# Kernel tuning notes

Measured on AMD Instinct MI355X. Metric: run time of the kernel, lower is better.

The kernel has to match this reference:

```python
import jax, jax.numpy as jnp
import numpy as np

B, S, H = 4, 8192, 1024


def setup_inputs() -> dict:
    key = jax.random.key(0)
    kq, kk, kv, k1, k2, k3, k4 = jax.random.split(key, 7)
    residual_init_factor = 1.0
    return {
        "q": jax.random.normal(kq, (B, S, H), dtype=jnp.float32),
        "k": jax.random.normal(kk, (B, S, H), dtype=jnp.float32),
        "v": jax.random.normal(kv, (B, S, H), dtype=jnp.float32),
        "w_q": 0.01 * jax.random.normal(k1, (H, H), dtype=jnp.float32),
        "w_k": 0.01 * jax.random.normal(k2, (H, H), dtype=jnp.float32),
        "w_v": 0.01 * jax.random.normal(k3, (H, H), dtype=jnp.float32),
        "w_p": 0.01 * residual_init_factor * jax.random.normal(k4, (H, H), dtype=jnp.float32),
    }


def reference(q, k, v, w_q, w_k, w_v, w_p):
    # Projections: [B,S,H] @ [H,H]
    emb_q = jnp.einsum("bsh,hd->bsd", q, w_q)
    emb_k = jnp.einsum("bsh,hd->bsd", k, w_k)
    emb_v = jnp.einsum("bsh,hd->bsd", v, w_v)
    # AFT-simple: per-channel exponential-weighted causal prefix average
    k_exp = jnp.exp(emb_k)
    k_exp_prefix = jnp.cumsum(k_exp, axis=1)
    k_exp_v_prefix = jnp.cumsum(k_exp * emb_v, axis=1)
    y = jax.nn.sigmoid(emb_q) * (k_exp_v_prefix / k_exp_prefix)
    return jnp.einsum("bsh,hd->bsd", y, w_p)
```

## Files before the change

kernel.cpp:

```cpp
#include <hip/hip_runtime.h>
#include <hip/hip_bf16.h>
#include <cstdint>

#define AS_GLOBAL __attribute__((address_space(1)))
#define AS_LDS    __attribute__((address_space(3)))

typedef __attribute__((ext_vector_type(8))) short bf16x8;
typedef __attribute__((ext_vector_type(8))) unsigned short u16x8;
typedef __attribute__((ext_vector_type(4))) float f32x4;

static __device__ __forceinline__ ushort f2bf(float x) {
    union { float f; uint32_t u; } c;
    c.f = x;
    uint32_t u = c.u;
    u += 0x7fffu + ((u >> 16) & 1u);
    return (ushort)(u >> 16);
}
static __device__ __forceinline__ float bf2f(ushort u) {
    union { uint32_t i; float f; } c;
    c.i = ((uint32_t)u) << 16;
    return c.f;
}

static __device__ __forceinline__ void gload_lds16(const void* g, void* l) {
    __builtin_amdgcn_global_load_lds(
        (const AS_GLOBAL uint32_t*)(uintptr_t)g,
        (AS_LDS uint32_t*)(uint32_t)(uintptr_t)l,
        16, 0, 0);
}

__global__ __launch_bounds__(256)
void cvt_f32_bf16(const float4* __restrict__ in, u16x8* __restrict__ out, int n8) {
    int i = blockIdx.x * 256 + threadIdx.x;
    int stride = gridDim.x * 256;
    for (; i < n8; i += stride) {
        float4 a = in[i * 2], b = in[i * 2 + 1];
        u16x8 o;
        o[0] = f2bf(a.x); o[1] = f2bf(a.y); o[2] = f2bf(a.z); o[3] = f2bf(a.w);
        o[4] = f2bf(b.x); o[5] = f2bf(b.y); o[6] = f2bf(b.z); o[7] = f2bf(b.w);
        out[i] = o;
    }
}

__global__ __launch_bounds__(256)
void transpose4_to_bf16(const float* __restrict__ w0, const float* __restrict__ w1,
                        const float* __restrict__ w2, const float* __restrict__ w3,
                        ushort* __restrict__ t0, ushort* __restrict__ t1,
                        ushort* __restrict__ t2, ushort* __restrict__ t3) {
    const int K = 1024, N = 1024;
    __shared__ float tile[32][33];
    const float* w; ushort* wt;
    switch (blockIdx.z) {
        case 0: w = w0; wt = t0; break;
        case 1: w = w1; wt = t1; break;
        case 2: w = w2; wt = t2; break;
        default: w = w3; wt = t3; break;
    }
    int bn = blockIdx.x * 32;
    int bk = blockIdx.y * 32;
    int tx = threadIdx.x & 31, ty = threadIdx.x >> 5;
    #pragma unroll
    for (int i = 0; i < 32; i += 8)
        tile[ty + i][tx] = w[(size_t)(bk + ty + i) * N + bn + tx];
    __syncthreads();
    #pragma unroll
    for (int i = 0; i < 32; i += 8)
        wt[(size_t)(bn + ty + i) * K + bk + tx] = f2bf(tile[tx][ty + i]);
}

template<int EPI, int OUT_BF>
__global__ __launch_bounds__(512, 2)
void gemm8p(const ushort* __restrict__ A, const ushort* __restrict__ Bt,
            void* __restrict__ Cv) {
    constexpr int K = 1024, N = 1024;
    __shared__ alignas(16) ushort sA[3][256 * 64];
    __shared__ alignas(16) ushort sB[3][128 * 64];
    const int tid  = threadIdx.x;
    const int wid  = tid >> 6;
    const int lane = tid & 63;
    const int wr = wid >> 1, wc = wid & 1;
    const int lr = lane & 15;
    const int kb = lane >> 4;
    const int x7 = lr & 7;

    const int wg = blockIdx.x;
    const int xcd = wg & 7, local = wg >> 3;
    const int bm = xcd * 16 + (local >> 3);
    const int bn = local & 7;
    const int m0 = bm * 256, n0 = bn * 128;

    f32x4 acc[4][4] = {};
    bf16x8 af[4][2];
    bf16x8 bv[2][2];

    auto stageA2 = [&](int tile, int buf, int j0) {
        const int kt0 = tile * 64;
        #pragma unroll
        for (int j = 0; j < 2; j++) {
            int c = (j0 + j) * 512 + tid;
            int r = c >> 3, p = c & 7;
            int s = p ^ (r & 7);
            gload_lds16(A + (size_t)(m0 + r) * K + kt0 + s * 8, &sA[buf][c * 8]);
        }
    };
    auto stageB1 = [&](int tile, int buf, int j) {
        const int kt0 = tile * 64;
        int c = j * 512 + tid;
        int r = c >> 3, p = c & 7;
        int s = p ^ (r & 7);
        gload_lds16(Bt + (size_t)(n0 + r) * K + kt0 + s * 8, &sB[buf][c * 8]);
    };
    auto readA = [&](int buf) {
        #pragma unroll
        for (int m = 0; m < 4; m++)
            #pragma unroll
            for (int kh = 0; kh < 2; kh++)
                af[m][kh] = *(const bf16x8*)&sA[buf][(wr * 64 + m * 16 + lr) * 64
                                                    + ((kh * 4 + kb) ^ x7) * 8];
    };
    auto readB = [&](int buf, int nq) {
        #pragma unroll
        for (int n = 0; n < 2; n++)
            #pragma unroll
            for (int kh = 0; kh < 2; kh++)
                bv[n][kh] = *(const bf16x8*)&sB[buf][(wc * 64 + nq * 32 + n * 16 + lr) * 64
                                                    + ((kh * 4 + kb) ^ x7) * 8];
    };
    auto mfma16 = [&](int nq) {
        #pragma unroll
        for (int m = 0; m < 4; m++)
            #pragma unroll
            for (int n = 0; n < 2; n++) {
                acc[m][nq * 2 + n] = __builtin_amdgcn_mfma_f32_16x16x32_bf16(
                    af[m][0], bv[n][0], acc[m][nq * 2 + n], 0, 0, 0);
                acc[m][nq * 2 + n] = __builtin_amdgcn_mfma_f32_16x16x32_bf16(
                    af[m][1], bv[n][1], acc[m][nq * 2 + n], 0, 0, 0);
            }
    };

    stageA2(0, 0, 0); stageA2(0, 0, 2); stageB1(0, 0, 0); stageB1(0, 0, 1);
    stageA2(1, 1, 0); stageA2(1, 1, 2); stageB1(1, 1, 0); stageB1(1, 1, 1);
    asm volatile("s_waitcnt vmcnt(6)" ::: "memory");
    __builtin_amdgcn_s_barrier();
    asm volatile("" ::: "memory");

    for (int t = 0; t < 16; t++) {
        const int b  = t % 3;
        const int b2 = (t + 2) % 3;
        const bool st = (t < 14);
        readA(b);
        readB(b, 0);
        if (st) { stageA2(t + 2, b2, 0); stageB1(t + 2, b2, 0); }
        asm volatile("" ::: "memory");
        __builtin_amdgcn_s_barrier();
        asm volatile("s_waitcnt lgkmcnt(0)" ::: "memory");
        __builtin_amdgcn_s_setprio(1);
        mfma16(0);
        __builtin_amdgcn_s_setprio(0);
        asm volatile("" ::: "memory");
        __builtin_amdgcn_s_barrier();
        asm volatile("" ::: "memory");
        readB(b, 1);
        if (st) { stageA2(t + 2, b2, 2); stageB1(t + 2, b2, 1); }
        asm volatile("" ::: "memory");
        __builtin_amdgcn_s_barrier();
        asm volatile("s_waitcnt lgkmcnt(0)" ::: "memory");
        __builtin_amdgcn_s_setprio(1);
        mfma16(1);
        __builtin_amdgcn_s_setprio(0);
        if (t < 14)       asm volatile("s_waitcnt vmcnt(6)" ::: "memory");
        else if (t == 14) asm volatile("s_waitcnt vmcnt(0)" ::: "memory");
        asm volatile("" ::: "memory");
        __builtin_amdgcn_s_barrier();
        asm volatile("" ::: "memory");
    }

    float*  Cf = (float*)Cv;
    ushort* Cb = (ushort*)Cv;
    #pragma unroll
    for (int m = 0; m < 4; m++) {
        #pragma unroll
        for (int n = 0; n < 4; n++) {
            #pragma unroll
            for (int r = 0; r < 4; r++) {
                int row = m0 + wr * 64 + m * 16 + (lane >> 4) * 4 + r;
                int col = n0 + wc * 64 + n * 16 + (lane & 15);
                float v = acc[m][n][r];
                if (EPI == 1) v = 1.0f / (1.0f + __expf(-v));
                else if (EPI == 2) v = __expf(v);
                size_t idx = (size_t)row * N + col;
                if (OUT_BF) Cb[idx] = f2bf(v);
                else        Cf[idx] = v;
            }
        }
    }
}

__global__ __launch_bounds__(256)
void scan_partials(const ushort* __restrict__ ke, const ushort* __restrict__ ev,
                   float* __restrict__ pke, float* __restrict__ pkv) {
    const int H = 1024, S = 8192, CHUNK = 32, BH = 4096;
    int c  = blockIdx.x * 2 + (threadIdx.x >> 7);
    int h0 = (threadIdx.x & 127) * 8;
    int b  = blockIdx.y;
    size_t base = ((size_t)b * S + (size_t)c * CHUNK) * H + h0;
    float se[8] = {}, sv[8] = {};
    for (int s = 0; s < CHUNK; s++) {
        u16x8 e8 = *(const u16x8*)(ke + base + (size_t)s * H);
        u16x8 v8 = *(const u16x8*)(ev + base + (size_t)s * H);
        #pragma unroll
        for (int i = 0; i < 8; i++) {
            float e = bf2f(e8[i]);
            se[i] += e;
            sv[i] += e * bf2f(v8[i]);
        }
    }
    size_t p = (size_t)c * BH + b * H + h0;
    *(float4*)(pke + p)     = make_float4(se[0], se[1], se[2], se[3]);
    *(float4*)(pke + p + 4) = make_float4(se[4], se[5], se[6], se[7]);
    *(float4*)(pkv + p)     = make_float4(sv[0], sv[1], sv[2], sv[3]);
    *(float4*)(pkv + p + 4) = make_float4(sv[4], sv[5], sv[6], sv[7]);
}

__global__ __launch_bounds__(256)
void scan_offsets(float* __restrict__ pke, float* __restrict__ pkv, int nch, int BH) {
    int i = blockIdx.x * blockDim.x + threadIdx.x;
    if (i >= BH) return;
    float rke = 0.f, rkv = 0.f;
    #pragma unroll 8
    for (int c = 0; c < nch; c++) {
        size_t idx = (size_t)c * BH + i;
        float a = pke[idx], b = pkv[idx];
        pke[idx] = rke; pkv[idx] = rkv;
        rke += a; rkv += b;
    }
}

__global__ __launch_bounds__(256)
void scan_final(const ushort* __restrict__ ke, const ushort* __restrict__ ev,
                const ushort* __restrict__ sq,
                const float* __restrict__ pke, const float* __restrict__ pkv,
                ushort* __restrict__ ybf) {
    const int H = 1024, S = 8192, CHUNK = 32, BH = 4096;
    int c  = blockIdx.x * 2 + (threadIdx.x >> 7);
    int h0 = (threadIdx.x & 127) * 8;
    int b  = blockIdx.y;
    size_t p = (size_t)c * BH + b * H + h0;
    float rke[8], rkv[8];
    *(float4*)(rke)     = *(const float4*)(pke + p);
    *(float4*)(rke + 4) = *(const float4*)(pke + p + 4);
    *(float4*)(rkv)     = *(const float4*)(pkv + p);
    *(float4*)(rkv + 4) = *(const float4*)(pkv + p + 4);
    size_t base = ((size_t)b * S + (size_t)c * CHUNK) * H + h0;
    for (int s = 0; s < CHUNK; s++) {
        size_t idx = base + (size_t)s * H;
        u16x8 e8 = *(const u16x8*)(ke + idx);
        u16x8 v8 = *(const u16x8*)(ev + idx);
        u16x8 q8 = *(const u16x8*)(sq + idx);
        u16x8 o;
        #pragma unroll
        for (int i = 0; i < 8; i++) {
            float e = bf2f(e8[i]);
            rke[i] += e;
            rkv[i] += e * bf2f(v8[i]);
            o[i] = f2bf(bf2f(q8[i]) * (rkv[i] / rke[i]));
        }
        *(u16x8*)(ybf + idx) = o;
    }
}

extern "C" void kernel_launch(void* const* d_in, const int* in_sizes, int n_in,
                              void* d_out, int out_size, void* d_ws, size_t ws_size,
                              hipStream_t stream) {
    const float* q   = (const float*)d_in[0];
    const float* k   = (const float*)d_in[1];
    const float* v   = (const float*)d_in[2];
    const float* w_q = (const float*)d_in[3];
    const float* w_k = (const float*)d_in[4];
    const float* w_v = (const float*)d_in[5];
    const float* w_p = (const float*)d_in[6];
    float* out = (float*)d_out;

    const int B = 4, S = 8192, H = 1024;
    const int M = B * S;
    const size_t MH = (size_t)M * H;
    const int NCH = 256;
    const int BH = B * H;

    char* ws = (char*)d_ws;
    size_t off = 0;
    auto alloc = [&](size_t bytes) -> char* {
        char* p = ws + off;
        off += (bytes + 255) & ~(size_t)255;
        return p;
    };
    ushort* abuf = (ushort*)alloc(MH * 2);
    ushort* wqt  = (ushort*)alloc((size_t)H * H * 2);
    ushort* wkt  = (ushort*)alloc((size_t)H * H * 2);
    ushort* wvt  = (ushort*)alloc((size_t)H * H * 2);
    ushort* wpt  = (ushort*)alloc((size_t)H * H * 2);
    ushort* sqb  = (ushort*)alloc(MH * 2);
    ushort* keb  = (ushort*)alloc(MH * 2);
    ushort* evb  = (ushort*)alloc(MH * 2);
    float*  pke  = (float*)alloc((size_t)NCH * BH * 4);
    float*  pkv  = (float*)alloc((size_t)NCH * BH * 4);

    const int ngg = (M / 256) * (H / 128);
    dim3 tg(H / 32, H / 32, 4);
    dim3 gs(NCH / 2, B);
    const int n8 = (int)(MH / 8);

    transpose4_to_bf16<<<tg, 256, 0, stream>>>(w_q, w_k, w_v, w_p, wqt, wkt, wvt, wpt);

    cvt_f32_bf16<<<2048, 256, 0, stream>>>((const float4*)q, (u16x8*)abuf, n8);
    gemm8p<1, 1><<<ngg, 512, 0, stream>>>(abuf, wqt, sqb);
    cvt_f32_bf16<<<2048, 256, 0, stream>>>((const float4*)k, (u16x8*)abuf, n8);
    gemm8p<2, 1><<<ngg, 512, 0, stream>>>(abuf, wkt, keb);
    cvt_f32_bf16<<<2048, 256, 0, stream>>>((const float4*)v, (u16x8*)abuf, n8);
    gemm8p<0, 1><<<ngg, 512, 0, stream>>>(abuf, wvt, evb);

    scan_partials<<<gs, 256, 0, stream>>>(keb, evb, pke, pkv);
    scan_offsets<<<BH / 256, 256, 0, stream>>>(pke, pkv, NCH, BH);
    scan_final<<<gs, 256, 0, stream>>>(keb, evb, sqb, pke, pkv, abuf);

    gemm8p<0, 0><<<ngg, 512, 0, stream>>>(abuf, wpt, out);
}
```

Before: 553.8 us.

## Enlarge GEMM block tile to 256x256 with 8-phase double-buffered pipeline

The GEMM block tile grows from 256x128 to 256x256. Each wave now computes a 128x64 output tile with 128 accumulator registers, and the 3-stage LDS ring becomes a 2-stage double buffer organised as quarter tiles. Eight interleaved phases alternate A and B half-tile loads with MFMA work. The aim is to raise arithmetic intensity and cut the number of global and LDS loads per FLOP, at the cost of much higher register pressure (possible spills or lower occupancy with launch_bounds 512,2) and fewer blocks (512 per GEMM).

New measurement: 530.1 us. -4.3%, faster.

```diff
diff --git a/kernel.cpp b/kernel.cpp
--- a/kernel.cpp
+++ b/kernel.cpp
@@ -73,119 +73,151 @@
 void gemm8p(const ushort* __restrict__ A, const ushort* __restrict__ Bt,
             void* __restrict__ Cv) {
     constexpr int K = 1024, N = 1024;
-    __shared__ alignas(16) ushort sA[3][256 * 64];
-    __shared__ alignas(16) ushort sB[3][128 * 64];
+    __shared__ alignas(16) ushort sA[2][16384];
+    __shared__ alignas(16) ushort sB[2][16384];
     const int tid  = threadIdx.x;
     const int wid  = tid >> 6;
     const int lane = tid & 63;
-    const int wr = wid >> 1, wc = wid & 1;
+    const int wr = wid >> 2, wc = wid & 3;
     const int lr = lane & 15;
     const int kb = lane >> 4;
     const int x7 = lr & 7;
 
     const int wg = blockIdx.x;
     const int xcd = wg & 7, local = wg >> 3;
-    const int bm = xcd * 16 + (local >> 3);
-    const int bn = local & 7;
-    const int m0 = bm * 256, n0 = bn * 128;
-
-    f32x4 acc[4][4] = {};
+    const int bm = xcd * 16 + (local >> 2);
+    const int bn = local & 3;
+    const int m0 = bm * 256, n0 = bn * 256;
+
+    f32x4 acc[8][4] = {};
     bf16x8 af[4][2];
-    bf16x8 bv[2][2];
-
-    auto stageA2 = [&](int tile, int buf, int j0) {
+    bf16x8 bv0[2][2], bv1[2][2];
+
+    auto stageA = [&](int tile, int buf, int mh) {
         const int kt0 = tile * 64;
         #pragma unroll
         for (int j = 0; j < 2; j++) {
-            int c = (j0 + j) * 512 + tid;
-            int r = c >> 3, p = c & 7;
-            int s = p ^ (r & 7);
-            gload_lds16(A + (size_t)(m0 + r) * K + kt0 + s * 8, &sA[buf][c * 8]);
-        }
-    };
-    auto stageB1 = [&](int tile, int buf, int j) {
+            int c = j * 512 + tid;
+            int rl = c >> 3, p = c & 7;
+            int s = p ^ (rl & 7);
+            int gr = (rl >> 6) * 128 + mh * 64 + (rl & 63);
+            gload_lds16(A + (size_t)(m0 + gr) * K + kt0 + s * 8,
+                        &sA[buf][mh * 8192 + c * 8]);
+        }
+    };
+    auto stageB = [&](int tile, int buf, int nh) {
         const int kt0 = tile * 64;
-        int c = j * 512 + tid;
-        int r = c >> 3, p = c & 7;
-        int s = p ^ (r & 7);
-        gload_lds16(Bt + (size_t)(n0 + r) * K + kt0 + s * 8, &sB[buf][c * 8]);
-    };
-    auto readA = [&](int buf) {
+        #pragma unroll
+        for (int j = 0; j < 2; j++) {
+            int c = j * 512 + tid;
+            int cl = c >> 3, p = c & 7;
+            int s = p ^ (cl & 7);
+            int gc = (cl >> 5) * 64 + nh * 32 + (cl & 31);
+            gload_lds16(Bt + (size_t)(n0 + gc) * K + kt0 + s * 8,
+                        &sB[buf][nh * 8192 + c * 8]);
+        }
+    };
+    auto readA = [&](int buf, int mq) {
         #pragma unroll
         for (int m = 0; m < 4; m++)
             #pragma unroll
             for (int kh = 0; kh < 2; kh++)
-                af[m][kh] = *(const bf16x8*)&sA[buf][(wr * 64 + m * 16 + lr) * 64
-                                                    + ((kh * 4 + kb) ^ x7) * 8];
-    };
-    auto readB = [&](int buf, int nq) {
+                af[m][kh] = *(const bf16x8*)&sA[buf][mq * 8192
+                              + (wr * 64 + m * 16 + lr) * 64
+                              + ((kh * 4 + kb) ^ x7) * 8];
+    };
+    auto readB = [&](bf16x8 (&dst)[2][2], int buf, int nq) {
         #pragma unroll
         for (int n = 0; n < 2; n++)
             #pragma unroll
             for (int kh = 0; kh < 2; kh++)
-                bv[n][kh] = *(const bf16x8*)&sB[buf][(wc * 64 + nq * 32 + n * 16 + lr) * 64
-                                                    + ((kh * 4 + kb) ^ x7) * 8];
-    };
-    auto mfma16 = [&](int nq) {
+                dst[n][kh] = *(const bf16x8*)&sB[buf][nq * 8192
+                              + (wc * 32 + n * 16 + lr) * 64
+                              + ((kh * 4 + kb) ^ x7) * 8];
+    };
+    auto mfma16 = [&](bf16x8 (&BV)[2][2], int mq, int nq) {
         #pragma unroll
         for (int m = 0; m < 4; m++)
             #pragma unroll
             for (int n = 0; n < 2; n++) {
-                acc[m][nq * 2 + n] = __builtin_amdgcn_mfma_f32_16x16x32_bf16(
-                    af[m][0], bv[n][0], acc[m][nq * 2 + n], 0, 0, 0);
-                acc[m][nq * 2 + n] = __builtin_amdgcn_mfma_f32_16x16x32_bf16(
-                    af[m][1], bv[n][1], acc[m][nq * 2 + n], 0, 0, 0);
+                acc[mq*4+m][nq*2+n] = __builtin_amdgcn_mfma_f32_16x16x32_bf16(
+                    af[m][0], BV[n][0], acc[mq*4+m][nq*2+n], 0, 0, 0);
+                acc[mq*4+m][nq*2+n] = __builtin_amdgcn_mfma_f32_16x16x32_bf16(
+                    af[m][1], BV[n][1], acc[mq*4+m][nq*2+n], 0, 0, 0);
             }
     };
 
-    stageA2(0, 0, 0); stageA2(0, 0, 2); stageB1(0, 0, 0); stageB1(0, 0, 1);
-    stageA2(1, 1, 0); stageA2(1, 1, 2); stageB1(1, 1, 0); stageB1(1, 1, 1);
-    asm volatile("s_waitcnt vmcnt(6)" ::: "memory");
+#define PHASE(BV, MQ, NQ, READS, STAGES, ENDW) { \
+    READS \
+    STAGES \
+    asm volatile("" ::: "memory"); \
+    __builtin_amdgcn_s_barrier(); \
+    asm volatile("s_waitcnt lgkmcnt(0)" ::: "memory"); \
+    __builtin_amdgcn_s_setprio(1); \
+    mfma16(BV, MQ, NQ); \
+    __builtin_amdgcn_s_setprio(0); \
+    ENDW \
+    asm volatile("" ::: "memory"); \
+    __builtin_amdgcn_s_barrier(); \
+    asm volatile("" ::: "memory"); \
+}
+
+    stageA(0, 0, 0); stageA(0, 0, 1); stageB(0, 0, 0); stageB(0, 0, 1);
+    stageA(1, 1, 0); stageA(1, 1, 1); stageB(1, 1, 0); stageB(1, 1, 1);
+    asm volatile("s_waitcnt vmcnt(0)" ::: "memory");
     __builtin_amdgcn_s_barrier();
     asm volatile("" ::: "memory");
 
-    for (int t = 0; t < 16; t++) {
-        const int b  = t % 3;
-        const int b2 = (t + 2) % 3;
-        const bool st = (t < 14);
-        readA(b);
-        readB(b, 0);
-        if (st) { stageA2(t + 2, b2, 0); stageB1(t + 2, b2, 0); }
-        asm volatile("" ::: "memory");
-        __builtin_amdgcn_s_barrier();
-        asm volatile("s_waitcnt lgkmcnt(0)" ::: "memory");
-        __builtin_amdgcn_s_setprio(1);
-        mfma16(0);
-        __builtin_amdgcn_s_setprio(0);
-        asm volatile("" ::: "memory");
-        __builtin_amdgcn_s_barrier();
-        asm volatile("" ::: "memory");
-        readB(b, 1);
-        if (st) { stageA2(t + 2, b2, 2); stageB1(t + 2, b2, 1); }
-        asm volatile("" ::: "memory");
-        __builtin_amdgcn_s_barrier();
-        asm volatile("s_waitcnt lgkmcnt(0)" ::: "memory");
-        __builtin_amdgcn_s_setprio(1);
-        mfma16(1);
-        __builtin_amdgcn_s_setprio(0);
-        if (t < 14)       asm volatile("s_waitcnt vmcnt(6)" ::: "memory");
-        else if (t == 14) asm volatile("s_waitcnt vmcnt(0)" ::: "memory");
-        asm volatile("" ::: "memory");
-        __builtin_amdgcn_s_barrier();
-        asm volatile("" ::: "memory");
-    }
+    for (int i = 0; i < 8; i++) {
+        const int t = 2 * i;
+        const int bt = t & 1, bt1 = bt ^ 1;
+        PHASE(bv0, 0, 0,
+            { readA(bt, 0); readB(bv0, bt, 0); },
+            { if (i > 0) stageA(t + 1, bt1, 0); },
+            { })
+        PHASE(bv1, 0, 1,
+            { readB(bv1, bt, 1); },
+            { if (i > 0) stageA(t + 1, bt1, 1); },
+            { asm volatile("s_waitcnt vmcnt(8)" ::: "memory"); })
+        PHASE(bv0, 1, 0,
+            { readA(bt, 1); },
+            { if (i < 7) stageB(t + 2, bt, 0); },
+            { })
+        PHASE(bv1, 1, 1,
+            { },
+            { if (i < 7) stageB(t + 2, bt, 1); },
+            { if (i < 7) asm volatile("s_waitcnt vmcnt(6)" ::: "memory");
+              else       asm volatile("s_waitcnt vmcnt(0)" ::: "memory"); })
+        PHASE(bv0, 0, 0,
+            { readA(bt1, 0); readB(bv0, bt1, 0); },
+            { if (i < 7) stageA(t + 2, bt, 0); },
+            { })
+        PHASE(bv1, 0, 1,
+            { readB(bv1, bt1, 1); },
+            { if (i < 7) stageA(t + 2, bt, 1); },
+            { if (i < 7) asm volatile("s_waitcnt vmcnt(8)" ::: "memory"); })
+        PHASE(bv0, 1, 0,
+            { readA(bt1, 1); },
+            { if (i < 7) stageB(t + 3, bt1, 0); },
+            { })
+        PHASE(bv1, 1, 1,
+            { },
+            { if (i < 7) stageB(t + 3, bt1, 1); },
+            { if (i < 7) asm volatile("s_waitcnt vmcnt(6)" ::: "memory"); })
+    }
+#undef PHASE
 
     float*  Cf = (float*)Cv;
     ushort* Cb = (ushort*)Cv;
     #pragma unroll
-    for (int m = 0; m < 4; m++) {
-        #pragma unroll
-        for (int n = 0; n < 4; n++) {
+    for (int am = 0; am < 8; am++) {
+        #pragma unroll
+        for (int an = 0; an < 4; an++) {
             #pragma unroll
             for (int r = 0; r < 4; r++) {
-                int row = m0 + wr * 64 + m * 16 + (lane >> 4) * 4 + r;
-                int col = n0 + wc * 64 + n * 16 + (lane & 15);
-                float v = acc[m][n][r];
+                int row = m0 + wr * 128 + (am >> 2) * 64 + (am & 3) * 16 + (lane >> 4) * 4 + r;
+                int col = n0 + wc * 64 + (an >> 1) * 32 + (an & 1) * 16 + lr;
+                float v = acc[am][an][r];
                 if (EPI == 1) v = 1.0f / (1.0f + __expf(-v));
                 else if (EPI == 2) v = __expf(v);
                 size_t idx = (size_t)row * N + col;
@@ -305,7 +337,7 @@
     float*  pke  = (float*)alloc((size_t)NCH * BH * 4);
     float*  pkv  = (float*)alloc((size_t)NCH * BH * 4);
 
-    const int ngg = (M / 256) * (H / 128);
+    const int ngg = (M / 256) * (H / 256);
     dim3 tg(H / 32, H / 32, 4);
     dim3 gs(NCH / 2, B);
     const int n8 = (int)(MH / 8);
```
